# Optimization experiments

Hardware: AMD Instinct MI355X
Metric: run time of the kernel (lower is better)

Reference implementation:

```python
import jax, jax.numpy as jnp
import numpy as np

N = 100000      # nodes
E = 3200000     # edges (avg degree 32, undirected)
FIN = 256
FOUT = 256
K = 4


def setup_inputs() -> dict:
    key = jax.random.key(0)
    k1, k2, k3 = jax.random.split(key, 3)
    x = jax.random.normal(k1, (N, FIN), dtype=jnp.float32)
    edge_index = jax.random.randint(k2, (2, E), 0, N, dtype=jnp.int32)
    stdv = 1.0 / np.sqrt(FIN * K)
    # K per-hop dense projection weights, uniform(-stdv, stdv) as in reset_parameters
    weights = jax.random.uniform(k3, (K, FIN, FOUT), dtype=jnp.float32,
                                 minval=-stdv, maxval=stdv)
    return {"x": x, "edge_index": edge_index, "weights": weights}


def reference(x, edge_index, weights):
    # edge_index -> symmetric adjacency S (from_edgelist builds an undirected graph):
    # spmm(S, z)[i] = sum over neighbors j of z[j]; scatter-add both directions.
    src, dst = edge_index[0], edge_index[1]

    def spmm(z):
        out = jnp.zeros_like(z).at[dst].add(z[src])
        return out.at[src].add(z[dst])

    zs = [x]
    for _ in range(1, weights.shape[0]):
        x = spmm(x)           # [N, Fin] k-hop diffused features
        zs.append(x)
    # sum_k zs[k] @ weights[k]  -> [N, Fout]
    return jnp.einsum('knf,kfo->no', jnp.stack(zs), weights)
```

## Files before the change

### kernel.cpp

```cpp
#include <hip/hip_runtime.h>
#include <hip/hip_bf16.h>


#define NNODES 100000
#define NEDGES 3200000
#define FINF   256
#define FOUTF  256
#define KTOT   1024
#define MPAD   100096
#define MTILES 782
#define NB     782
#define FILLB  1024
#define CHUNK  3125

typedef __attribute__((ext_vector_type(8))) short bf16x8;
typedef __attribute__((ext_vector_type(4))) float f32x4;

__device__ __forceinline__ unsigned short f2bf(float f) {
  unsigned int u = __float_as_uint(f);
  unsigned int r = (u + 0x7fffu + ((u >> 16) & 1u)) >> 16;
  return (unsigned short)r;
}

__device__ __forceinline__ void async_ld16(const void* g, void* l) {
  __builtin_amdgcn_global_load_lds(
      (const __attribute__((address_space(1))) unsigned int*)g,
      (__attribute__((address_space(3))) unsigned int*)l, 16, 0, 0);
}


__global__ __launch_bounds__(256)
void bucket_count_kernel(const int* __restrict__ ei, int* __restrict__ bcount) {
  __shared__ int h[NB];
  for (int i = threadIdx.x; i < NB; i += 256) h[i] = 0;
  __syncthreads();
  for (int e = blockIdx.x * 256 + threadIdx.x; e < NEDGES; e += gridDim.x * 256) {
    int s = ei[e];
    int d = ei[NEDGES + e];
    atomicAdd(&h[d >> 7], 1);
    atomicAdd(&h[s >> 7], 1);
  }
  __syncthreads();
  for (int i = threadIdx.x; i < NB; i += 256) {
    int c = h[i];
    if (c) atomicAdd(&bcount[i], c);
  }
}

__global__ __launch_bounds__(1024)
void bucket_scan_kernel(const int* __restrict__ bcount, int* __restrict__ bbase,
                        int* __restrict__ bcursor) {
  __shared__ int ws[16];
  int t = threadIdx.x, lane = t & 63, wv = t >> 6;
  int v = (t < NB) ? bcount[t] : 0;
  int s = v;
  #pragma unroll
  for (int off = 1; off < 64; off <<= 1) {
    int tmp = __shfl_up(s, off, 64);
    if (lane >= off) s += tmp;
  }
  if (lane == 63) ws[wv] = s;
  __syncthreads();
  if (t == 0) {
    int run = 0;
    #pragma unroll
    for (int k = 0; k < 16; ++k) { int tmp = ws[k]; ws[k] = run; run += tmp; }
  }
  __syncthreads();
  int excl = s + ws[wv] - v;
  if (t < NB) { bbase[t] = excl; bcursor[t] = excl; }
  if (t == NB) bbase[NB] = excl;
}

__global__ __launch_bounds__(256)
void bin_fill_kernel(const int* __restrict__ ei, int* __restrict__ bcursor,
                     unsigned long long* __restrict__ binned) {
  __shared__ int h[NB];
  for (int i = threadIdx.x; i < NB; i += 256) h[i] = 0;
  __syncthreads();
  const int e0 = blockIdx.x * CHUNK;
  const int e1 = (e0 + CHUNK < NEDGES) ? e0 + CHUNK : NEDGES;
  for (int e = e0 + threadIdx.x; e < e1; e += 256) {
    int s = ei[e];
    int d = ei[NEDGES + e];
    atomicAdd(&h[d >> 7], 1);
    atomicAdd(&h[s >> 7], 1);
  }
  __syncthreads();
  for (int i = threadIdx.x; i < NB; i += 256) {
    int c = h[i];
    h[i] = c ? atomicAdd(&bcursor[i], c) : 0;
  }
  __syncthreads();
  for (int e = e0 + threadIdx.x; e < e1; e += 256) {
    int s = ei[e];
    int d = ei[NEDGES + e];
    int p = atomicAdd(&h[d >> 7], 1);
    binned[p] = ((unsigned long long)d << 32) | (unsigned int)s;
    int q = atomicAdd(&h[s >> 7], 1);
    binned[q] = ((unsigned long long)s << 32) | (unsigned int)d;
  }
}

__global__ __launch_bounds__(256)
void bucket_csr_kernel(const unsigned long long* __restrict__ binned,
                       const int* __restrict__ bbase,
                       int* __restrict__ row_ptr, int* __restrict__ adj) {
  __shared__ int cnt[128];
  __shared__ int cur[128];
  const int b = blockIdx.x;
  const int node0 = b << 7;
  const int base = bbase[b];
  const int end = bbase[b + 1];
  const int tid = threadIdx.x;
  if (tid < 128) cnt[tid] = 0;
  __syncthreads();
  for (int i = base + tid; i < end; i += 256) {
    unsigned long long v = binned[i];
    int owner = (int)(v >> 32);
    atomicAdd(&cnt[owner - node0], 1);
  }
  __syncthreads();
  if (tid < 128) {
    int ex = 0;
    #pragma unroll 8
    for (int j = 0; j < 128; ++j) {
      int c = cnt[j];
      ex += (j < tid) ? c : 0;
    }
    int node = node0 + tid;
    if (node < NNODES) row_ptr[node] = base + ex;
    cur[tid] = base + ex;
  }
  if (tid == 0 && b == NB - 1) row_ptr[NNODES] = end;
  __syncthreads();
  for (int i = base + tid; i < end; i += 256) {
    unsigned long long v = binned[i];
    int owner = (int)(v >> 32);
    int nbr = (int)(v & 0xffffffffu);
    int p = atomicAdd(&cur[owner - node0], 1);
    adj[p] = nbr << 8;
  }
}


__global__ __launch_bounds__(256)
void convert_x_kernel(const float* __restrict__ x,
                      unsigned short* __restrict__ z,
                      unsigned char* __restrict__ g0,
                      float* __restrict__ sc0) {
  const int row = (blockIdx.x * 256 + threadIdx.x) >> 6;
  const int lane = threadIdx.x & 63;
  if (row >= NNODES) return;
  float4 xv = *(const float4*)&x[(size_t)row * FINF + (lane << 2)];

  ushort4 o;
  o.x = f2bf(xv.x); o.y = f2bf(xv.y); o.z = f2bf(xv.z); o.w = f2bf(xv.w);
  *(ushort4*)&z[(size_t)row * KTOT + (lane << 2)] = o;

  float m = fmaxf(fmaxf(fabsf(xv.x), fabsf(xv.y)), fmaxf(fabsf(xv.z), fabsf(xv.w)));
  #pragma unroll
  for (int i = 1; i < 64; i <<= 1) m = fmaxf(m, __shfl_xor(m, i, 64));
  float inv = (m > 0.f) ? 127.f / m : 0.f;
  unsigned int q0 = (unsigned int)__builtin_rintf(__builtin_fmaf(xv.x, inv, 128.f));
  unsigned int q1 = (unsigned int)__builtin_rintf(__builtin_fmaf(xv.y, inv, 128.f));
  unsigned int q2 = (unsigned int)__builtin_rintf(__builtin_fmaf(xv.z, inv, 128.f));
  unsigned int q3 = (unsigned int)__builtin_rintf(__builtin_fmaf(xv.w, inv, 128.f));
  *(unsigned int*)(g0 + (size_t)row * 256 + (lane << 2)) =
      q0 | (q1 << 8) | (q2 << 16) | (q3 << 24);
  if (lane == 0) sc0[row] = m * (1.f / 127.f);
}

__global__ void zero_pad_kernel(unsigned short* __restrict__ z) {
  size_t row = NNODES + blockIdx.x;
  *(ushort4*)&z[row * KTOT + (threadIdx.x << 2)] = make_ushort4(0, 0, 0, 0);
}

__global__ void convert_w_kernel(const float* __restrict__ w, unsigned short* __restrict__ Bt) {
  int idx = blockIdx.x * 256 + threadIdx.x;
  int o = idx >> 10, kk = idx & 1023;
  Bt[idx] = f2bf(w[(size_t)kk * FOUTF + o]);
}


#define DECQ(vv, ss)                                        \
  { acc0 += (ss) * (float)((vv) & 255u);                    \
    acc1 += (ss) * (float)(((vv) >> 8) & 255u);             \
    acc2 += (ss) * (float)(((vv) >> 16) & 255u);            \
    acc3 += (ss) * (float)((vv) >> 24);                     \
    ssum += (ss); }

__global__ __launch_bounds__(256)
void spmm_q8_kernel(const unsigned char* __restrict__ gin,
                    const float* __restrict__ sin,
                    unsigned char* __restrict__ gout,
                    float* __restrict__ sout,
                    unsigned short* __restrict__ zslot,
                    const int* __restrict__ row_ptr,
                    const int* __restrict__ adjb) {
  const int wid = (blockIdx.x * 256 + threadIdx.x) >> 6;
  const int lane = threadIdx.x & 63;
  if (wid >= NNODES) return;
  const int beg = row_ptr[wid];
  const int end = row_ptr[wid + 1];
  const int lb = lane << 2;
  const char* scb = (const char*)sin;

  float acc0 = 0.f, acc1 = 0.f, acc2 = 0.f, acc3 = 0.f, ssum = 0.f;
  int j = beg;
  for (; j + 4 <= end; j += 4) {
    int o0 = adjb[j + 0], o1 = adjb[j + 1], o2 = adjb[j + 2], o3 = adjb[j + 3];
    float s0 = *(const float*)(scb + (o0 >> 6));
    float s1 = *(const float*)(scb + (o1 >> 6));
    float s2 = *(const float*)(scb + (o2 >> 6));
    float s3 = *(const float*)(scb + (o3 >> 6));
    unsigned int v0 = *(const unsigned int*)(gin + o0 + lb);
    unsigned int v1 = *(const unsigned int*)(gin + o1 + lb);
    unsigned int v2 = *(const unsigned int*)(gin + o2 + lb);
    unsigned int v3 = *(const unsigned int*)(gin + o3 + lb);
    DECQ(v0, s0); DECQ(v1, s1); DECQ(v2, s2); DECQ(v3, s3);
  }
  for (; j < end; ++j) {
    int o = adjb[j];
    float s = *(const float*)(scb + (o >> 6));
    unsigned int v = *(const unsigned int*)(gin + o + lb);
    DECQ(v, s);
  }

  const float bias = 128.f * ssum;
  const float a0 = acc0 - bias;
  const float a1 = acc1 - bias;
  const float a2 = acc2 - bias;
  const float a3 = acc3 - bias;

  uint2 ob;
  ob.x = (unsigned int)f2bf(a0) | ((unsigned int)f2bf(a1) << 16);
  ob.y = (unsigned int)f2bf(a2) | ((unsigned int)f2bf(a3) << 16);
  *(uint2*)((char*)zslot + ((size_t)wid << 11) + (lane << 3)) = ob;

  if (gout) {
    float m = fmaxf(fmaxf(fabsf(a0), fabsf(a1)), fmaxf(fabsf(a2), fabsf(a3)));
    #pragma unroll
    for (int i = 1; i < 64; i <<= 1) m = fmaxf(m, __shfl_xor(m, i, 64));
    float inv = (m > 0.f) ? 127.f / m : 0.f;
    unsigned int q0 = (unsigned int)__builtin_rintf(__builtin_fmaf(a0, inv, 128.f));
    unsigned int q1 = (unsigned int)__builtin_rintf(__builtin_fmaf(a1, inv, 128.f));
    unsigned int q2 = (unsigned int)__builtin_rintf(__builtin_fmaf(a2, inv, 128.f));
    unsigned int q3 = (unsigned int)__builtin_rintf(__builtin_fmaf(a3, inv, 128.f));
    *(unsigned int*)(gout + (size_t)wid * 256 + lb) =
        q0 | (q1 << 8) | (q2 << 16) | (q3 << 24);
    if (lane == 0) sout[wid] = m * (1.f / 127.f);
  }
}


__global__ __launch_bounds__(256)
void gemm_kernel(const unsigned short* __restrict__ A,
                 const unsigned short* __restrict__ Bt,
                 float* __restrict__ C) {
  __shared__ __align__(16) unsigned short As[128 * 32];
  __shared__ __align__(16) unsigned short Bs[128 * 32];
  const int tid = threadIdx.x;
  const int lane = tid & 63;
  const int wave = tid >> 6;
  const int bm = blockIdx.x >> 1;
  const int bn = blockIdx.x & 1;
  const int wr = wave >> 1, wc = wave & 1;

  const int rowA_base = bm * 128;
  const int colB_base = bn * 128;
  const int sub_r = lane >> 2;
  const int kp = (lane & 3) << 3;

  f32x4 acc[4][4] = {};

  for (int k0 = 0; k0 < KTOT; k0 += 32) {
    __syncthreads();
    #pragma unroll
    for (int i = 0; i < 2; ++i) {
      int chunk = i * 4 + wave;
      int row = chunk * 16 + sub_r;
      const unsigned short* ga = A + (size_t)(rowA_base + row) * KTOT + k0 + kp;
      async_ld16(ga, &As[chunk * 512]);
      const unsigned short* gb = Bt + (size_t)(colB_base + row) * KTOT + k0 + kp;
      async_ld16(gb, &Bs[chunk * 512]);
    }
    __syncthreads();

    bf16x8 a[4], b[4];
    #pragma unroll
    for (int m = 0; m < 4; ++m)
      a[m] = *(const bf16x8*)&As[(wr * 64 + m * 16 + (lane & 15)) * 32 + (lane >> 4) * 8];
    #pragma unroll
    for (int n = 0; n < 4; ++n)
      b[n] = *(const bf16x8*)&Bs[(wc * 64 + n * 16 + (lane & 15)) * 32 + (lane >> 4) * 8];
    #pragma unroll
    for (int m = 0; m < 4; ++m) {
      #pragma unroll
      for (int n = 0; n < 4; ++n)
        acc[m][n] = __builtin_amdgcn_mfma_f32_16x16x32_bf16(a[m], b[n], acc[m][n], 0, 0, 0);
    }
  }

  const int ccol0 = colB_base + wc * 64 + (lane & 15);
  const int crow0 = rowA_base + wr * 64 + ((lane >> 4) << 2);
  #pragma unroll
  for (int m = 0; m < 4; ++m) {
    #pragma unroll
    for (int j = 0; j < 4; ++j) {
      int r = crow0 + m * 16 + j;
      if (r < NNODES) {
        float* cp = C + (size_t)r * FOUTF + ccol0;
        #pragma unroll
        for (int n = 0; n < 4; ++n) cp[n * 16] = acc[m][n][j];
      }
    }
  }
}


extern "C" void kernel_launch(void* const* d_in, const int* in_sizes, int n_in,
                              void* d_out, int out_size, void* d_ws, size_t ws_size,
                              hipStream_t stream) {
  (void)in_sizes; (void)n_in; (void)out_size; (void)ws_size;
  const float* x  = (const float*)d_in[0];
  const int*   ei = (const int*)d_in[1];
  const float* w  = (const float*)d_in[2];
  float* out = (float*)d_out;

  char* ws = (char*)d_ws;
  size_t off = 0;
  auto carve = [&](size_t bytes) -> void* {
    void* p = ws + off;
    off = (off + bytes + 255) & ~(size_t)255;
    return p;
  };
  unsigned short* z  = (unsigned short*)carve((size_t)MPAD * KTOT * 2);
  unsigned short* Bt = (unsigned short*)carve((size_t)FOUTF * KTOT * 2);
  int* row_ptr       = (int*)carve((size_t)(NNODES + 1) * 4);
  int* adj           = (int*)carve((size_t)2 * NEDGES * 4);
  int* bcount        = (int*)carve((size_t)(NB + 1) * 4);
  int* bbase         = (int*)carve((size_t)(NB + 1) * 4);
  int* bcursor       = (int*)carve((size_t)(NB + 1) * 4);
  unsigned char* gA  = (unsigned char*)carve((size_t)NNODES * 256);
  unsigned char* gB  = (unsigned char*)carve((size_t)NNODES * 256);
  float* scA         = (float*)carve((size_t)NNODES * 4);
  float* scB         = (float*)carve((size_t)NNODES * 4);
  unsigned long long* binned = (unsigned long long*)z;

  hipMemsetAsync(bcount, 0, (size_t)(NB + 1) * 4, stream);

  bucket_count_kernel<<<1024, 256, 0, stream>>>(ei, bcount);
  bucket_scan_kernel<<<1, 1024, 0, stream>>>(bcount, bbase, bcursor);
  bin_fill_kernel<<<FILLB, 256, 0, stream>>>(ei, bcursor, binned);
  bucket_csr_kernel<<<NB, 256, 0, stream>>>(binned, bbase, row_ptr, adj);

  convert_x_kernel<<<25000, 256, 0, stream>>>(x, z, gA, scA);
  zero_pad_kernel<<<MPAD - NNODES, 256, 0, stream>>>(z);
  convert_w_kernel<<<1024, 256, 0, stream>>>(w, Bt);

  spmm_q8_kernel<<<25000, 256, 0, stream>>>(gA, scA, gB, scB, z + 1 * FINF,
                                            row_ptr, adj);
  spmm_q8_kernel<<<25000, 256, 0, stream>>>(gB, scB, gA, scA, z + 2 * FINF,
                                            row_ptr, adj);
  spmm_q8_kernel<<<25000, 256, 0, stream>>>(gA, scA, (unsigned char*)nullptr,
                                            (float*)nullptr, z + 3 * FINF,
                                            row_ptr, adj);

  gemm_kernel<<<MTILES * 2, 256, 0, stream>>>(z, Bt, out);
}
```

Measured before the change: 1.032 ms.

## Replace bf16 GEMM with int8 MFMA GEMM on per-row quantized hop features

Each hop's features are now stored only as signed int8 with per-row scales, and the weights are quantized to int8 with a per-hop scale. The final projection becomes an int8 MFMA GEMM that rescales the int32 partial sums per hop, in place of the bf16 GEMM over a 1024-wide concatenated matrix. This drops the bf16 feature writes and halves the GEMM input bytes, and binned edges are packed into 32-bit words instead of 64-bit. The cost is larger quantization error in both the features and the weights, which risks failing tolerance, plus one extra SpMM output buffer.

```diff
diff --git a/kernel.cpp b/kernel.cpp
--- a/kernel.cpp
+++ b/kernel.cpp
@@ -4,23 +4,15 @@
 
 #define NNODES 100000
 #define NEDGES 3200000
-#define FINF   256
 #define FOUTF  256
-#define KTOT   1024
 #define MPAD   100096
 #define MTILES 782
 #define NB     782
 #define FILLB  1024
 #define CHUNK  3125
 
-typedef __attribute__((ext_vector_type(8))) short bf16x8;
+typedef __attribute__((ext_vector_type(4))) int   i32x4;
 typedef __attribute__((ext_vector_type(4))) float f32x4;
-
-__device__ __forceinline__ unsigned short f2bf(float f) {
-  unsigned int u = __float_as_uint(f);
-  unsigned int r = (u + 0x7fffu + ((u >> 16) & 1u)) >> 16;
-  return (unsigned short)r;
-}
 
 __device__ __forceinline__ void async_ld16(const void* g, void* l) {
   __builtin_amdgcn_global_load_lds(
@@ -74,7 +66,7 @@
 
 __global__ __launch_bounds__(256)
 void bin_fill_kernel(const int* __restrict__ ei, int* __restrict__ bcursor,
-                     unsigned long long* __restrict__ binned) {
+                     unsigned int* __restrict__ binned) {
   __shared__ int h[NB];
   for (int i = threadIdx.x; i < NB; i += 256) h[i] = 0;
   __syncthreads();
@@ -96,14 +88,14 @@
     int s = ei[e];
     int d = ei[NEDGES + e];
     int p = atomicAdd(&h[d >> 7], 1);
-    binned[p] = ((unsigned long long)d << 32) | (unsigned int)s;
+    binned[p] = ((unsigned int)(d & 127) << 17) | (unsigned int)s;
     int q = atomicAdd(&h[s >> 7], 1);
-    binned[q] = ((unsigned long long)s << 32) | (unsigned int)d;
-  }
-}
-
-__global__ __launch_bounds__(256)
-void bucket_csr_kernel(const unsigned long long* __restrict__ binned,
+    binned[q] = ((unsigned int)(s & 127) << 17) | (unsigned int)d;
+  }
+}
+
+__global__ __launch_bounds__(256)
+void bucket_csr_kernel(const unsigned int* __restrict__ binned,
                        const int* __restrict__ bbase,
                        int* __restrict__ row_ptr, int* __restrict__ adj) {
   __shared__ int cnt[128];
@@ -116,9 +108,8 @@
   if (tid < 128) cnt[tid] = 0;
   __syncthreads();
   for (int i = base + tid; i < end; i += 256) {
-    unsigned long long v = binned[i];
-    int owner = (int)(v >> 32);
-    atomicAdd(&cnt[owner - node0], 1);
+    unsigned int v = binned[i];
+    atomicAdd(&cnt[v >> 17], 1);
   }
   __syncthreads();
   if (tid < 128) {
@@ -135,10 +126,9 @@
   if (tid == 0 && b == NB - 1) row_ptr[NNODES] = end;
   __syncthreads();
   for (int i = base + tid; i < end; i += 256) {
-    unsigned long long v = binned[i];
-    int owner = (int)(v >> 32);
-    int nbr = (int)(v & 0xffffffffu);
-    int p = atomicAdd(&cur[owner - node0], 1);
+    unsigned int v = binned[i];
+    int nbr = (int)(v & 0x1FFFFu);
+    int p = atomicAdd(&cur[v >> 17], 1);
     adj[p] = nbr << 8;
   }
 }
@@ -146,40 +136,50 @@
 
 __global__ __launch_bounds__(256)
 void convert_x_kernel(const float* __restrict__ x,
-                      unsigned short* __restrict__ z,
                       unsigned char* __restrict__ g0,
                       float* __restrict__ sc0) {
   const int row = (blockIdx.x * 256 + threadIdx.x) >> 6;
   const int lane = threadIdx.x & 63;
   if (row >= NNODES) return;
-  float4 xv = *(const float4*)&x[(size_t)row * FINF + (lane << 2)];
-
-  ushort4 o;
-  o.x = f2bf(xv.x); o.y = f2bf(xv.y); o.z = f2bf(xv.z); o.w = f2bf(xv.w);
-  *(ushort4*)&z[(size_t)row * KTOT + (lane << 2)] = o;
+  float4 xv = *(const float4*)&x[(size_t)row * 256 + (lane << 2)];
 
   float m = fmaxf(fmaxf(fabsf(xv.x), fabsf(xv.y)), fmaxf(fabsf(xv.z), fabsf(xv.w)));
   #pragma unroll
   for (int i = 1; i < 64; i <<= 1) m = fmaxf(m, __shfl_xor(m, i, 64));
   float inv = (m > 0.f) ? 127.f / m : 0.f;
-  unsigned int q0 = (unsigned int)__builtin_rintf(__builtin_fmaf(xv.x, inv, 128.f));
-  unsigned int q1 = (unsigned int)__builtin_rintf(__builtin_fmaf(xv.y, inv, 128.f));
-  unsigned int q2 = (unsigned int)__builtin_rintf(__builtin_fmaf(xv.z, inv, 128.f));
-  unsigned int q3 = (unsigned int)__builtin_rintf(__builtin_fmaf(xv.w, inv, 128.f));
+  int q0 = (int)__builtin_rintf(xv.x * inv);
+  int q1 = (int)__builtin_rintf(xv.y * inv);
+  int q2 = (int)__builtin_rintf(xv.z * inv);
+  int q3 = (int)__builtin_rintf(xv.w * inv);
   *(unsigned int*)(g0 + (size_t)row * 256 + (lane << 2)) =
-      q0 | (q1 << 8) | (q2 << 16) | (q3 << 24);
+      ((unsigned)q0 & 255u) | (((unsigned)q1 & 255u) << 8) |
+      (((unsigned)q2 & 255u) << 16) | (((unsigned)q3 & 255u) << 24);
   if (lane == 0) sc0[row] = m * (1.f / 127.f);
 }
 
-__global__ void zero_pad_kernel(unsigned short* __restrict__ z) {
-  size_t row = NNODES + blockIdx.x;
-  *(ushort4*)&z[row * KTOT + (threadIdx.x << 2)] = make_ushort4(0, 0, 0, 0);
-}
-
-__global__ void convert_w_kernel(const float* __restrict__ w, unsigned short* __restrict__ Bt) {
+__global__ void wmax_kernel(const float* __restrict__ w, float* __restrict__ dW) {
+  __shared__ float red[4];
+  const int k = blockIdx.x;
+  const float* wk = w + (size_t)k * 65536;
+  float m = 0.f;
+  for (int i = threadIdx.x; i < 65536; i += 256) m = fmaxf(m, fabsf(wk[i]));
+  #pragma unroll
+  for (int i = 1; i < 64; i <<= 1) m = fmaxf(m, __shfl_xor(m, i, 64));
+  if ((threadIdx.x & 63) == 0) red[threadIdx.x >> 6] = m;
+  __syncthreads();
+  if (threadIdx.x == 0) {
+    m = fmaxf(fmaxf(red[0], red[1]), fmaxf(red[2], red[3]));
+    dW[k] = m * (1.f / 127.f);
+    dW[4 + k] = (m > 0.f) ? 127.f / m : 0.f;
+  }
+}
+
+__global__ void quantw_kernel(const float* __restrict__ w, const float* __restrict__ dW,
+                              signed char* __restrict__ W8) {
   int idx = blockIdx.x * 256 + threadIdx.x;
-  int o = idx >> 10, kk = idx & 1023;
-  Bt[idx] = f2bf(w[(size_t)kk * FOUTF + o]);
+  int k = idx >> 16, o = (idx >> 8) & 255, f = idx & 255;
+  float inv = dW[4 + k];
+  W8[idx] = (signed char)(int)__builtin_rintf(w[(size_t)(k * 256 + f) * 256 + o] * inv);
 }
 
 
@@ -195,10 +195,9 @@
                     const float* __restrict__ sin,
                     unsigned char* __restrict__ gout,
                     float* __restrict__ sout,
-                    unsigned short* __restrict__ zslot,
                     const int* __restrict__ row_ptr,
                     const int* __restrict__ adjb) {
-  const int wid = (blockIdx.x * 256 + threadIdx.x) >> 6;
+  const int wid = __builtin_amdgcn_readfirstlane((blockIdx.x * 256 + threadIdx.x) >> 6);
   const int lane = threadIdx.x & 63;
   if (wid >= NNODES) return;
   const int beg = row_ptr[wid];
@@ -214,16 +213,16 @@
     float s1 = *(const float*)(scb + (o1 >> 6));
     float s2 = *(const float*)(scb + (o2 >> 6));
     float s3 = *(const float*)(scb + (o3 >> 6));
-    unsigned int v0 = *(const unsigned int*)(gin + o0 + lb);
-    unsigned int v1 = *(const unsigned int*)(gin + o1 + lb);
-    unsigned int v2 = *(const unsigned int*)(gin + o2 + lb);
-    unsigned int v3 = *(const unsigned int*)(gin + o3 + lb);
+    unsigned int v0 = *(const unsigned int*)(gin + o0 + lb) ^ 0x80808080u;
+    unsigned int v1 = *(const unsigned int*)(gin + o1 + lb) ^ 0x80808080u;
+    unsigned int v2 = *(const unsigned int*)(gin + o2 + lb) ^ 0x80808080u;
+    unsigned int v3 = *(const unsigned int*)(gin + o3 + lb) ^ 0x80808080u;
     DECQ(v0, s0); DECQ(v1, s1); DECQ(v2, s2); DECQ(v3, s3);
   }
   for (; j < end; ++j) {
     int o = adjb[j];
     float s = *(const float*)(scb + (o >> 6));
-    unsigned int v = *(const unsigned int*)(gin + o + lb);
+    unsigned int v = *(const unsigned int*)(gin + o + lb) ^ 0x80808080u;
     DECQ(v, s);
   }
 
@@ -233,76 +232,94 @@
   const float a2 = acc2 - bias;
   const float a3 = acc3 - bias;
 
-  uint2 ob;
-  ob.x = (unsigned int)f2bf(a0) | ((unsigned int)f2bf(a1) << 16);
-  ob.y = (unsigned int)f2bf(a2) | ((unsigned int)f2bf(a3) << 16);
-  *(uint2*)((char*)zslot + ((size_t)wid << 11) + (lane << 3)) = ob;
-
-  if (gout) {
-    float m = fmaxf(fmaxf(fabsf(a0), fabsf(a1)), fmaxf(fabsf(a2), fabsf(a3)));
-    #pragma unroll
-    for (int i = 1; i < 64; i <<= 1) m = fmaxf(m, __shfl_xor(m, i, 64));
-    float inv = (m > 0.f) ? 127.f / m : 0.f;
-    unsigned int q0 = (unsigned int)__builtin_rintf(__builtin_fmaf(a0, inv, 128.f));
-    unsigned int q1 = (unsigned int)__builtin_rintf(__builtin_fmaf(a1, inv, 128.f));
-    unsigned int q2 = (unsigned int)__builtin_rintf(__builtin_fmaf(a2, inv, 128.f));
-    unsigned int q3 = (unsigned int)__builtin_rintf(__builtin_fmaf(a3, inv, 128.f));
-    *(unsigned int*)(gout + (size_t)wid * 256 + lb) =
-        q0 | (q1 << 8) | (q2 << 16) | (q3 << 24);
-    if (lane == 0) sout[wid] = m * (1.f / 127.f);
-  }
-}
-
-
-__global__ __launch_bounds__(256)
-void gemm_kernel(const unsigned short* __restrict__ A,
-                 const unsigned short* __restrict__ Bt,
-                 float* __restrict__ C) {
-  __shared__ __align__(16) unsigned short As[128 * 32];
-  __shared__ __align__(16) unsigned short Bs[128 * 32];
+  float m = fmaxf(fmaxf(fabsf(a0), fabsf(a1)), fmaxf(fabsf(a2), fabsf(a3)));
+  #pragma unroll
+  for (int i = 1; i < 64; i <<= 1) m = fmaxf(m, __shfl_xor(m, i, 64));
+  float inv = (m > 0.f) ? 127.f / m : 0.f;
+  int q0 = (int)__builtin_rintf(a0 * inv);
+  int q1 = (int)__builtin_rintf(a1 * inv);
+  int q2 = (int)__builtin_rintf(a2 * inv);
+  int q3 = (int)__builtin_rintf(a3 * inv);
+  *(unsigned int*)(gout + (size_t)wid * 256 + lb) =
+      ((unsigned)q0 & 255u) | (((unsigned)q1 & 255u) << 8) |
+      (((unsigned)q2 & 255u) << 16) | (((unsigned)q3 & 255u) << 24);
+  if (lane == 0) sout[wid] = m * (1.f / 127.f);
+}
+
+
+__global__ __launch_bounds__(512)
+void gemm_i8_kernel(const unsigned char* __restrict__ q0p,
+                    const unsigned char* __restrict__ q1p,
+                    const unsigned char* __restrict__ q2p,
+                    const unsigned char* __restrict__ q3p,
+                    const float* __restrict__ s0p,
+                    const float* __restrict__ s1p,
+                    const float* __restrict__ s2p,
+                    const float* __restrict__ s3p,
+                    const signed char* __restrict__ W8,
+                    const float* __restrict__ dW,
+                    float* __restrict__ C) {
+  __shared__ __align__(16) unsigned char As[128 * 64];
+  __shared__ __align__(16) unsigned char Bs[256 * 64];
   const int tid = threadIdx.x;
   const int lane = tid & 63;
   const int wave = tid >> 6;
-  const int bm = blockIdx.x >> 1;
-  const int bn = blockIdx.x & 1;
-  const int wr = wave >> 1, wc = wave & 1;
-
-  const int rowA_base = bm * 128;
-  const int colB_base = bn * 128;
-  const int sub_r = lane >> 2;
-  const int kp = (lane & 3) << 3;
-
-  f32x4 acc[4][4] = {};
-
-  for (int k0 = 0; k0 < KTOT; k0 += 32) {
-    __syncthreads();
-    #pragma unroll
-    for (int i = 0; i < 2; ++i) {
-      int chunk = i * 4 + wave;
-      int row = chunk * 16 + sub_r;
-      const unsigned short* ga = A + (size_t)(rowA_base + row) * KTOT + k0 + kp;
-      async_ld16(ga, &As[chunk * 512]);
-      const unsigned short* gb = Bt + (size_t)(colB_base + row) * KTOT + k0 + kp;
-      async_ld16(gb, &Bs[chunk * 512]);
+  const int wr = wave >> 2;
+  const int wc = wave & 3;
+  const int rowA_base = blockIdx.x * 128;
+
+  const unsigned char* qs[4] = {q0p, q1p, q2p, q3p};
+  const float* scs[4] = {s0p, s1p, s2p, s3p};
+
+  const int st_row = tid >> 2;
+  const int st_kb = (tid & 3) << 4;
+
+  f32x4 accf[4][4] = {};
+
+  #pragma unroll
+  for (int k = 0; k < 4; ++k) {
+    const unsigned char* Qk = qs[k];
+    const signed char* Wk = W8 + (size_t)k * 65536;
+    i32x4 acci[4][4] = {};
+    for (int k0 = 0; k0 < 256; k0 += 64) {
+      __syncthreads();
+      async_ld16(Qk + (size_t)(rowA_base + st_row) * 256 + k0 + st_kb,
+                 &As[st_row * 64 + st_kb]);
+      async_ld16(Wk + (size_t)st_row * 256 + k0 + st_kb,
+                 &Bs[st_row * 64 + st_kb]);
+      async_ld16(Wk + (size_t)(128 + st_row) * 256 + k0 + st_kb,
+                 &Bs[(128 + st_row) * 64 + st_kb]);
+      __syncthreads();
+      i32x4 a[4], b[4];
+      #pragma unroll
+      for (int m = 0; m < 4; ++m)
+        a[m] = *(const i32x4*)&As[(wr * 64 + m * 16 + (lane & 15)) * 64 + (lane >> 4) * 16];
+      #pragma unroll
+      for (int n = 0; n < 4; ++n)
+        b[n] = *(const i32x4*)&Bs[(wc * 64 + n * 16 + (lane & 15)) * 64 + (lane >> 4) * 16];
+      #pragma unroll
+      for (int m = 0; m < 4; ++m) {
+        #pragma unroll
+        for (int n = 0; n < 4; ++n)
+          acci[m][n] = __builtin_amdgcn_mfma_i32_16x16x64_i8(a[m], b[n], acci[m][n], 0, 0, 0);
+      }
     }
-    __syncthreads();
-
-    bf16x8 a[4], b[4];
-    #pragma unroll
-    for (int m = 0; m < 4; ++m)
-      a[m] = *(const bf16x8*)&As[(wr * 64 + m * 16 + (lane & 15)) * 32 + (lane >> 4) * 8];
-    #pragma unroll
-    for (int n = 0; n < 4; ++n)
-      b[n] = *(const bf16x8*)&Bs[(wc * 64 + n * 16 + (lane & 15)) * 32 + (lane >> 4) * 8];
+    const float dWk = dW[k];
+    const float* sk = scs[k];
     #pragma unroll
     for (int m = 0; m < 4; ++m) {
       #pragma unroll
-      for (int n = 0; n < 4; ++n)
-        acc[m][n] = __builtin_amdgcn_mfma_f32_16x16x32_bf16(a[m], b[n], acc[m][n], 0, 0, 0);
+      for (int j = 0; j < 4; ++j) {
+        int r = rowA_base + wr * 64 + ((lane >> 4) << 2) + m * 16 + j;
+        float s = sk[r] * dWk;
+        #pragma unroll
+        for (int n = 0; n < 4; ++n)
+          accf[m][n][j] += s * (float)acci[m][n][j];
+      }
     }
   }
 
-  const int ccol0 = colB_base + wc * 64 + (lane & 15);
+  const int ccol0 = wc * 64 + (lane & 15);
   const int crow0 = rowA_base + wr * 64 + ((lane >> 4) << 2);
   #pragma unroll
   for (int m = 0; m < 4; ++m) {
@@ -312,7 +329,7 @@
       if (r < NNODES) {
         float* cp = C + (size_t)r * FOUTF + ccol0;
         #pragma unroll
-        for (int n = 0; n < 4; ++n) cp[n * 16] = acc[m][n][j];
+        for (int n = 0; n < 4; ++n) cp[n * 16] = accf[m][n][j];
       }
     }
   }
@@ -335,18 +352,22 @@
     off = (off + bytes + 255) & ~(size_t)255;
     return p;
   };
-  unsigned short* z  = (unsigned short*)carve((size_t)MPAD * KTOT * 2);
-  unsigned short* Bt = (unsigned short*)carve((size_t)FOUTF * KTOT * 2);
-  int* row_ptr       = (int*)carve((size_t)(NNODES + 1) * 4);
-  int* adj           = (int*)carve((size_t)2 * NEDGES * 4);
-  int* bcount        = (int*)carve((size_t)(NB + 1) * 4);
-  int* bbase         = (int*)carve((size_t)(NB + 1) * 4);
-  int* bcursor       = (int*)carve((size_t)(NB + 1) * 4);
-  unsigned char* gA  = (unsigned char*)carve((size_t)NNODES * 256);
-  unsigned char* gB  = (unsigned char*)carve((size_t)NNODES * 256);
-  float* scA         = (float*)carve((size_t)NNODES * 4);
-  float* scB         = (float*)carve((size_t)NNODES * 4);
-  unsigned long long* binned = (unsigned long long*)z;
+  unsigned char* gA = (unsigned char*)carve((size_t)MPAD * 256);
+  unsigned char* gB = (unsigned char*)carve((size_t)MPAD * 256);
+  unsigned char* gC = (unsigned char*)carve((size_t)MPAD * 256);
+  unsigned char* gD = (unsigned char*)carve((size_t)MPAD * 256);
+  float* scA        = (float*)carve((size_t)MPAD * 4);
+  float* scB        = (float*)carve((size_t)MPAD * 4);
+  float* scC        = (float*)carve((size_t)MPAD * 4);
+  float* scD        = (float*)carve((size_t)MPAD * 4);
+  signed char* W8   = (signed char*)carve((size_t)4 * 65536);
+  float* dW         = (float*)carve(8 * 4);
+  int* row_ptr      = (int*)carve((size_t)(NNODES + 1) * 4);
+  int* adj          = (int*)carve((size_t)2 * NEDGES * 4);
+  int* bcount       = (int*)carve((size_t)(NB + 1) * 4);
+  int* bbase        = (int*)carve((size_t)(NB + 1) * 4);
+  int* bcursor      = (int*)carve((size_t)(NB + 1) * 4);
+  unsigned int* binned = (unsigned int*)gD;
 
   hipMemsetAsync(bcount, 0, (size_t)(NB + 1) * 4, stream);
 
@@ -355,17 +376,14 @@
   bin_fill_kernel<<<FILLB, 256, 0, stream>>>(ei, bcursor, binned);
   bucket_csr_kernel<<<NB, 256, 0, stream>>>(binned, bbase, row_ptr, adj);
 
-  convert_x_kernel<<<25000, 256, 0, stream>>>(x, z, gA, scA);
-  zero_pad_kernel<<<MPAD - NNODES, 256, 0, stream>>>(z);
-  convert_w_kernel<<<1024, 256, 0, stream>>>(w, Bt);
-
-  spmm_q8_kernel<<<25000, 256, 0, stream>>>(gA, scA, gB, scB, z + 1 * FINF,
-                                            row_ptr, adj);
-  spmm_q8_kernel<<<25000, 256, 0, stream>>>(gB, scB, gA, scA, z + 2 * FINF,
-                                            row_ptr, adj);
-  spmm_q8_kernel<<<25000, 256, 0, stream>>>(gA, scA, (unsigned char*)nullptr,
-                                            (float*)nullptr, z + 3 * FINF,
-                                            row_ptr, adj);
-
-  gemm_kernel<<<MTILES * 2, 256, 0, stream>>>(z, Bt, out);
-}
+  convert_x_kernel<<<25000, 256, 0, stream>>>(x, gA, scA);
+  wmax_kernel<<<4, 256, 0, stream>>>(w, dW);
+  quantw_kernel<<<1024, 256, 0, stream>>>(w, dW, W8);
+
+  spmm_q8_kernel<<<25000, 256, 0, stream>>>(gA, scA, gB, scB, row_ptr, adj);
+  spmm_q8_kernel<<<25000, 256, 0, stream>>>(gB, scB, gC, scC, row_ptr, adj);
+  spmm_q8_kernel<<<25000, 256, 0, stream>>>(gC, scC, gD, scD, row_ptr, adj);
+
+  gemm_i8_kernel<<<MTILES, 512, 0, stream>>>(gA, gB, gC, gD, scA, scB, scC, scD,
+                                             W8, dW, out);
+}
```

Measured after the change: 1.087 ms. 1.05x slower.
